# Performance work log

Measured on AMD Instinct MI355X. Metric: run time of the kernel, lower is better.

The kernel has to match this reference:

```python
import jax, jax.numpy as jnp
import numpy as np

B = 36          # fixed batch_size in source
T = 60          # time_window
DECAY = 0.3     # LIAF default decay
THRESH = 0.5    # LIAF default firing threshold


def conv3x3(x, W, b):
    # x: [B,C,H,W], W: [O,C,3,3], padding=1, stride=1
    y = jax.lax.conv_general_dilated(x, W, (1, 1), [(1, 1), (1, 1)],
                                     dimension_numbers=('NCHW', 'OIHW', 'NCHW'))
    return y + b[None, :, None, None]


def avgpool2(x):
    # 2x2 average pool, stride 2
    b, c, h, w = x.shape
    return x.reshape(b, c, h // 2, 2, w // 2, 2).mean(axis=(3, 5))


def liaf(u, spike, mem):
    # leaky-integrate with spike-gated reset, analog (ReLU) fire
    mem = mem * DECAY * (1.0 - spike) + u
    new_spike = (mem > THRESH).astype(mem.dtype)
    out = jax.nn.relu(mem)
    return new_spike, mem, out


def setup_inputs() -> dict:
    key = jax.random.key(0)
    ks = jax.random.split(key, 8)
    # DVS event frames in [0,3) so the >1 binarization keeps ~2/3 of pixels
    data = (jax.random.uniform(ks[0], (B, 2, 32, 32, T)) * 3.0).astype(jnp.float32)

    def w(k, shape, fan_in):
        return (jax.random.normal(k, shape) * (1.0 / np.sqrt(fan_in))).astype(jnp.float32)

    return dict(
        data=data,
        win=T,
        W0=w(ks[1], (64, 2, 3, 3), 2 * 9), b0=jnp.zeros((64,), jnp.float32),
        W1=w(ks[2], (128, 64, 3, 3), 64 * 9), b1=jnp.zeros((128,), jnp.float32),
        W2=w(ks[3], (128, 128, 3, 3), 128 * 9), b2=jnp.zeros((128,), jnp.float32),
        Wf1=w(ks[4], (256, 8192), 8192), bf1=jnp.zeros((256,), jnp.float32),
        Wf2=w(ks[5], (11, 256), 256), bf2=jnp.zeros((11,), jnp.float32),
    )


def reference(data, W0, b0, W1, b1, W2, b2, Wf1, bf1, Wf2, bf2, win):
    dtype = data.dtype
    z = lambda s: jnp.zeros(s, dtype)
    # (spike, mem) pairs for every LIAF cell + output-spike accumulator
    state0 = (
        (z((B, 64, 32, 32)), z((B, 64, 32, 32))),   # c0
        (z((B, 128, 32, 32)), z((B, 128, 32, 32))), # c1
        (z((B, 128, 16, 16)), z((B, 128, 16, 16))), # p1
        (z((B, 128, 16, 16)), z((B, 128, 16, 16))), # c2
        (z((B, 128, 8, 8)), z((B, 128, 8, 8))),     # p2
        (z((B, 256)), z((B, 256))),                 # h1
        (z((B, 11)), z((B, 11))),                   # h2
        z((B, 11)),                                 # sum of analog outputs
    )
    xs = jnp.moveaxis(data, -1, 0)[:win]

    def step(st, xt):
        c0, c1, p1, c2, p2, h1, h2, acc = st
        x = (xt > 1.0).astype(dtype)  # binarize accumulated frame
        s, m, out = liaf(conv3x3(x, W0, b0), *c0); c0 = (s, m)
        s, m, out = liaf(conv3x3(out, W1, b1), *c1); c1 = (s, m)
        s, m, out = liaf(avgpool2(out), *p1); p1 = (s, m)
        s, m, out = liaf(conv3x3(out, W2, b2), *c2); c2 = (s, m)
        s, m, out = liaf(avgpool2(out), *p2); p2 = (s, m)
        out = out.reshape(B, -1)  # [B, 8*8*128]
        s, m, out = liaf(out @ Wf1.T + bf1, *h1); h1 = (s, m)
        s, m, out = liaf(out @ Wf2.T + bf2, *h2); h2 = (s, m)
        return (c0, c1, p1, c2, p2, h1, h2, acc + out), None

    st_f, _ = jax.lax.scan(step, state0, xs)
    return st_f[-1] / T
```

## Files before the change

kernel.cpp:

```cpp
#include <hip/hip_runtime.h>

#define NB 36
#define NT 60

typedef __attribute__((ext_vector_type(8))) short short8;
typedef __attribute__((ext_vector_type(4))) float f32x4;

struct Params {
  const float *data;
  const float *W0, *b0, *W1, *b1, *W2, *b2, *Wf1, *bf1, *Wf2, *bf2;
  float *xb, *w0t;
  unsigned short *w1h, *w1l, *w2h, *w2l;
  unsigned int *xhl, *p1hl;
  float *outp2, *u1s;
  float *dm0, *dm1, *dmp1, *dm2, *dmp2, *dmh1, *dmh2;
  float *acc;
  float *zbase; int zn4;
};

__device__ __forceinline__ unsigned short bf16_rne(float v){
  unsigned int bits = __float_as_uint(v);
  unsigned int r = bits + 0x7FFFu + ((bits >> 16) & 1u);
  return (unsigned short)(r >> 16);
}
__device__ __forceinline__ unsigned int bf16pack(float v){
  unsigned short h = bf16_rne(v);
  float hf = __uint_as_float((unsigned int)h << 16);
  unsigned short l = bf16_rne(v - hf);
  return (unsigned int)h | ((unsigned int)l << 16);
}
__device__ __forceinline__ void unpack8(const unsigned int* q, short8& h8, short8& l8){
  unsigned int u[8];
  *(uint4*)&u[0] = *(const uint4*)q;
  *(uint4*)&u[4] = *(const uint4*)(q+4);
  #pragma unroll
  for(int i=0;i<8;i++){
    h8[i] = (short)(u[i] & 0xffffu);
    l8[i] = (short)(u[i] >> 16);
  }
}

__global__ void __launch_bounds__(256) k_prep(Params p){
  int gt  = blockIdx.x*256 + threadIdx.x;
  int STR = gridDim.x*256;
  if(gt < NB*11) p.acc[gt] = 0.f;
  for(int i=gt; i<p.zn4; i+=STR) ((float4*)p.zbase)[i] = make_float4(0.f,0.f,0.f,0.f);
  const int PLANE = 34*34;
  for(int i=gt; i<NT*NB*2*PLANE; i+=STR){
    int t   = i / (NB*2*PLANE);
    int rem = i % (NB*2*PLANE);
    int bc  = rem / PLANE;
    int pix = rem % PLANE;
    int ph = pix/34, pw = pix%34;
    float v = 0.f;
    if(ph>=1 && ph<=32 && pw>=1 && pw<=32){
      float d = p.data[((size_t)bc*1024 + (ph-1)*32 + (pw-1))*NT + t];
      v = (d > 1.0f) ? 1.0f : 0.0f;
    }
    p.xb[i] = v;
  }
  for(int i=gt; i<2*9*64; i+=STR){
    int co=i%64, rr=i/64; p.w0t[i] = p.W0[(co*2 + rr/9)*9 + rr%9];
  }
  for(int i=gt; i<128*576; i+=STR){
    int co = i/576, k = i%576;
    int cin = k/9, dd = k%9;
    unsigned int pk = bf16pack(p.W1[(co*64+cin)*9 + dd]);
    p.w1h[i]=(unsigned short)(pk&0xffffu); p.w1l[i]=(unsigned short)(pk>>16);
  }
  for(int i=gt; i<128*1152; i+=STR){
    int co = i/1152, k = i%1152;
    int cin = k/9, dd = k%9;
    unsigned int pk = bf16pack(p.W2[(co*128+cin)*9 + dd]);
    p.w2h[i]=(unsigned short)(pk&0xffffu); p.w2l[i]=(unsigned short)(pk>>16);
  }
}

template<int Cin,int Cout,int HW,int CO,int PX,int TY,int CS>
__global__ void __launch_bounds__(HW*TY)
k_conv0(const float* __restrict__ x, const float* __restrict__ wt,
        const float* __restrict__ bias, float* __restrict__ dm,
        unsigned int* __restrict__ outhl,
        const float* __restrict__ u1s, const float* __restrict__ bf1,
        const float* __restrict__ Wf2, const float* __restrict__ bf2,
        float* __restrict__ dmh1, float* __restrict__ dmh2,
        float* __restrict__ accv, int do_fc2)
{
  const int NCOG = Cout/CO;
  const int TH   = PX*TY;
  const int NHG  = HW/TH;
  const int NH4  = CO/4;
  const int NTHL = HW*TY;
  const int PIN  = HW+2;
  const int XR   = PX+2;
  int tile = blockIdx.x;
  int tid  = threadIdx.x;

  __shared__ __align__(16) float wl[CS*9*CO];
  __shared__ float xs[256];

  if(do_fc2 && tile < NB){
    int b = tile;
    int o = tid;
    float u = bf1[o];
    const float* pu = u1s + (size_t)b*256 + o;
    #pragma unroll
    for(int s=0;s<32;s++) u += pu[(size_t)s*NB*256];
    int idx = b*256 + o;
    float mem = dmh1[idx] + u;
    float xo = mem > 0.f ? mem : 0.f;
    dmh1[idx] = (mem > 0.5f) ? 0.f : 0.3f*mem;
    xs[o] = xo;
    __syncthreads();
    int w2id = o >> 6, ln = o & 63;
    for(int oo=w2id; oo<11; oo+=4){
      const float* wr = Wf2 + oo*256;
      float s = xs[ln]*wr[ln] + xs[ln+64]*wr[ln+64]
              + xs[ln+128]*wr[ln+128] + xs[ln+192]*wr[ln+192];
      #pragma unroll
      for(int off=32; off>0; off>>=1) s += __shfl_down(s, off, 64);
      if(ln==0){
        int i2 = b*11 + oo;
        float m2 = dmh2[i2] + s + bf2[oo];
        float ov = m2 > 0.f ? m2 : 0.f;
        dmh2[i2] = (m2 > 0.5f) ? 0.f : 0.3f*m2;
        accv[i2] += ov * (1.0f/60.0f);
      }
    }
  }

  int cog = tile % NCOG;
  int hg  = (tile/NCOG) % NHG;
  int b   = tile/(NCOG*NHG);
  int w0  = tid % HW;
  int ty  = tid / HW;
  int h0  = hg*TH + ty*PX;

  float accs[PX][CO];
  #pragma unroll
  for(int p=0;p<PX;p++)
    #pragma unroll
    for(int c=0;c<CO;c++) accs[p][c]=0.f;

  for(int cs=0; cs<Cin; cs+=CS){
    __syncthreads();
    for(int j=tid; j<CS*9*CO; j+=NTHL){
      int c  = j % CO;
      int rr = j / CO;
      wl[j] = wt[(cs*9 + rr)*Cout + cog*CO + c];
    }
    __syncthreads();

    for(int lc=0; lc<CS; lc++){
      const float* xc = x + ((size_t)b*Cin + cs + lc)*PIN*PIN + (size_t)h0*PIN + w0;
      float xv[XR][3];
      #pragma unroll
      for(int r=0;r<XR;r++)
        #pragma unroll
        for(int c=0;c<3;c++) xv[r][c] = xc[(size_t)r*PIN + c];
      const float4* w4 = (const float4*)(wl + lc*9*CO);
      #pragma unroll
      for(int dh=0;dh<3;dh++){
        #pragma unroll
        for(int g=0;g<NH4;g++){
          float4 wa = w4[(dh*3+0)*NH4+g];
          float4 wb = w4[(dh*3+1)*NH4+g];
          float4 wc = w4[(dh*3+2)*NH4+g];
          const float* A  = (const float*)&wa;
          const float* Bp = (const float*)&wb;
          const float* Cp = (const float*)&wc;
          #pragma unroll
          for(int cc=0;cc<4;cc++){
            #pragma unroll
            for(int px=0;px<PX;px++)
              accs[px][g*4+cc] += A[cc]*xv[px+dh][0] + Bp[cc]*xv[px+dh][1] + Cp[cc]*xv[px+dh][2];
          }
        }
      }
    }
  }

  int co0 = cog*CO;
  #pragma unroll
  for(int co=0; co<CO; co++){
    float bsv = bias[co0+co];
    const int OS = HW + 2;
    size_t plane = (size_t)(b*Cout + co0+co)*OS*OS;
    #pragma unroll
    for(int px=0; px<PX; px++){
      size_t idx = plane + (size_t)(h0+px+1)*OS + w0 + 1;
      float mem = dm[idx] + accs[px][co] + bsv;
      float ov = mem > 0.f ? mem : 0.f;
      dm[idx]  = (mem > 0.5f) ? 0.f : 0.3f*mem;
      outhl[idx] = bf16pack(ov);
    }
  }
}

__global__ void __launch_bounds__(256)
k_conv1(const unsigned int* __restrict__ xhl,
        const unsigned short* __restrict__ w1h, const unsigned short* __restrict__ w1l,
        const float* __restrict__ bias, float* __restrict__ dm,
        float* __restrict__ dmp, unsigned int* __restrict__ p1hl)
{
  __shared__ __align__(16) unsigned int ldsu[8192];
  unsigned short* Ah = (unsigned short*)ldsu;
  unsigned short* Al = (unsigned short*)(ldsu + 1280);
  unsigned int*   Xp = ldsu + 2560;

  int bid = blockIdx.x;
  int cog = bid & 1;
  int pxg = (bid>>1) & 7;
  int b   = bid >> 4;
  int tid = threadIdx.x;
  int wv  = tid >> 6, lane = tid & 63;
  int wm = wv & 1, wn = wv >> 1;
  int n = lane & 15, quad = lane >> 4;
  int r0 = pxg*4;

  f32x4 acc[2][4];
  #pragma unroll
  for(int mo=0;mo<2;mo++)
    #pragma unroll
    for(int no=0;no<4;no++) acc[mo][no] = (f32x4){0.f,0.f,0.f,0.f};

  int aco = tid >> 2;
  int aq  = tid & 3;
  const unsigned short* whp = w1h + (size_t)(cog*64 + aco)*576 + aq*8;
  const unsigned short* wlp = w1l + (size_t)(cog*64 + aco)*576 + aq*8;
  int sk  = tid >> 3;
  int pxq = tid & 7;
  int srow = pxq >> 1;
  int scol = (pxq & 1) * 16;
  int pxb  = pxq * 16;
  int skx  = sk ^ ((pxq & 3) << 3);

  uint4 wha = *(const uint4*)(whp);
  uint4 wla = *(const uint4*)(wlp);
  unsigned int tmp[16];
  {
    int cin = sk / 9;
    int dd  = sk - cin*9;
    int dh = dd/3, dw = dd - dh*3;
    const unsigned int* sx = xhl + ((size_t)(b*64 + cin)*34 + (r0 + srow + dh))*34 + scol + dw;
    #pragma unroll
    for(int i=0;i<16;i++) tmp[i] = sx[i];
  }

  for(int ch=0; ch<18; ch++){
    __syncthreads();
    *(uint4*)&Ah[aco*40 + aq*8] = wha;
    *(uint4*)&Al[aco*40 + aq*8] = wla;
    #pragma unroll
    for(int i=0;i<16;i++) Xp[(pxb+i)*44 + skx] = tmp[i];
    __syncthreads();

    if(ch+1 < 18){
      int k0n = (ch+1)*32;
      wha = *(const uint4*)(whp + k0n);
      wla = *(const uint4*)(wlp + k0n);
      int kg = k0n + sk;
      int cin = kg / 9;
      int dd  = kg - cin*9;
      int dh = dd/3, dw = dd - dh*3;
      const unsigned int* sx = xhl + ((size_t)(b*64 + cin)*34 + (r0 + srow + dh))*34 + scol + dw;
      #pragma unroll
      for(int i=0;i<16;i++) tmp[i] = sx[i];
    }

    short8 ahf[2], alf[2];
    #pragma unroll
    for(int mo=0;mo<2;mo++){
      int row = wm*32 + mo*16 + n;
      ahf[mo] = *(const short8*)&Ah[row*40 + quad*8];
      alf[mo] = *(const short8*)&Al[row*40 + quad*8];
    }
    #pragma unroll
    for(int no=0;no<4;no++){
      int prow = wn*64 + no*16 + n;
      short8 xhf, xlf;
      unpack8(&Xp[prow*44 + ((quad ^ no) & 3)*8], xhf, xlf);
      #pragma unroll
      for(int mo=0;mo<2;mo++){
        acc[mo][no] = __builtin_amdgcn_mfma_f32_16x16x32_bf16(ahf[mo], xhf, acc[mo][no],0,0,0);
        acc[mo][no] = __builtin_amdgcn_mfma_f32_16x16x32_bf16(ahf[mo], xlf, acc[mo][no],0,0,0);
        acc[mo][no] = __builtin_amdgcn_mfma_f32_16x16x32_bf16(alf[mo], xhf, acc[mo][no],0,0,0);
      }
    }
  }

  #pragma unroll
  for(int mo=0;mo<2;mo++){
    #pragma unroll
    for(int reg=0;reg<4;reg++){
      int co = cog*64 + wm*32 + mo*16 + quad*4 + reg;
      float bsv = bias[co];
      float o[4];
      #pragma unroll
      for(int no=0;no<4;no++){
        int r = r0 + wn*2 + (no>>1);
        int c = (no&1)*16 + n;
        size_t idx = (((size_t)b*128 + co)*32 + r)*32 + c;
        float mem = dm[idx] + acc[mo][no][reg] + bsv;
        o[no] = mem > 0.f ? mem : 0.f;
        dm[idx] = (mem > 0.5f) ? 0.f : 0.3f*mem;
      }
      #pragma unroll
      for(int pp=0; pp<2; pp++){
        float s = o[pp] + o[pp+2];
        s += __shfl_xor(s, 1, 64);
        if((n&1)==0){
          int pr = pxg*2 + wn;
          int pc = pp*8 + (n>>1);
          size_t pidx = (((size_t)b*128 + co)*18 + pr+1)*18 + pc+1;
          float pm = dmp[pidx] + s*0.25f;
          float pv = pm > 0.f ? pm : 0.f;
          dmp[pidx] = (pm > 0.5f) ? 0.f : 0.3f*pm;
          p1hl[pidx] = bf16pack(pv);
        }
      }
    }
  }
}

__global__ void __launch_bounds__(256)
k_conv2(const unsigned int* __restrict__ xhl,
        const unsigned short* __restrict__ w2h, const unsigned short* __restrict__ w2l,
        const float* __restrict__ bias, float* __restrict__ dm,
        float* __restrict__ dmp, float* __restrict__ outp)
{
  __shared__ __align__(16) unsigned int ldsu[5376];
  unsigned short* Ah = (unsigned short*)ldsu;
  unsigned short* Al = (unsigned short*)(ldsu + 1280);
  unsigned int*   Xp = ldsu + 2560;

  int bid = blockIdx.x;
  int cog = bid & 1;
  int pxg = (bid>>1) & 3;
  int b   = bid >> 3;
  int tid = threadIdx.x;
  int wv  = tid >> 6, lane = tid & 63;
  int wm = wv & 1, wn = wv >> 1;
  int n = lane & 15, quad = lane >> 4;
  int r0 = pxg*4;

  f32x4 acc[2][2];
  #pragma unroll
  for(int mo=0;mo<2;mo++)
    #pragma unroll
    for(int no=0;no<2;no++) acc[mo][no] = (f32x4){0.f,0.f,0.f,0.f};

  int aco = tid >> 2;
  int aq  = tid & 3;
  const unsigned short* whp = w2h + (size_t)(cog*64 + aco)*1152 + aq*8;
  const unsigned short* wlp = w2l + (size_t)(cog*64 + aco)*1152 + aq*8;
  int sk  = tid >> 3;
  int pxq = tid & 7;
  int srow = pxq >> 1;
  int scol = (pxq & 1) * 8;
  int pxb  = pxq * 8;
  int skx  = sk ^ ((pxq >> 1) << 3);

  uint4 wha = *(const uint4*)(whp);
  uint4 wla = *(const uint4*)(wlp);
  unsigned int tmp[8];
  {
    int cin = sk / 9;
    int dd  = sk - cin*9;
    int dh = dd/3, dw = dd - dh*3;
    const unsigned int* sx = xhl + ((size_t)(b*128 + cin)*18 + (r0 + srow + dh))*18 + scol + dw;
    #pragma unroll
    for(int i=0;i<8;i++) tmp[i] = sx[i];
  }

  for(int ch=0; ch<36; ch++){
    __syncthreads();
    *(uint4*)&Ah[aco*40 + aq*8] = wha;
    *(uint4*)&Al[aco*40 + aq*8] = wla;
    #pragma unroll
    for(int i=0;i<8;i++) Xp[(pxb+i)*44 + skx] = tmp[i];
    __syncthreads();

    if(ch+1 < 36){
      int k0n = (ch+1)*32;
      wha = *(const uint4*)(whp + k0n);
      wla = *(const uint4*)(wlp + k0n);
      int kg = k0n + sk;
      int cin = kg / 9;
      int dd  = kg - cin*9;
      int dh = dd/3, dw = dd - dh*3;
      const unsigned int* sx = xhl + ((size_t)(b*128 + cin)*18 + (r0 + srow + dh))*18 + scol + dw;
      #pragma unroll
      for(int i=0;i<8;i++) tmp[i] = sx[i];
    }

    short8 ahf[2], alf[2];
    #pragma unroll
    for(int mo=0;mo<2;mo++){
      int row = wm*32 + mo*16 + n;
      ahf[mo] = *(const short8*)&Ah[row*40 + quad*8];
      alf[mo] = *(const short8*)&Al[row*40 + quad*8];
    }
    #pragma unroll
    for(int no=0;no<2;no++){
      int prow = wn*32 + no*16 + n;
      short8 xhf, xlf;
      unpack8(&Xp[prow*44 + ((quad ^ (wn*2 + no)) & 3)*8], xhf, xlf);
      #pragma unroll
      for(int mo=0;mo<2;mo++){
        acc[mo][no] = __builtin_amdgcn_mfma_f32_16x16x32_bf16(ahf[mo], xhf, acc[mo][no],0,0,0);
        acc[mo][no] = __builtin_amdgcn_mfma_f32_16x16x32_bf16(ahf[mo], xlf, acc[mo][no],0,0,0);
        acc[mo][no] = __builtin_amdgcn_mfma_f32_16x16x32_bf16(alf[mo], xhf, acc[mo][no],0,0,0);
      }
    }
  }

  #pragma unroll
  for(int mo=0;mo<2;mo++){
    #pragma unroll
    for(int reg=0;reg<4;reg++){
      int co = cog*64 + wm*32 + mo*16 + quad*4 + reg;
      float bsv = bias[co];
      float o[2];
      #pragma unroll
      for(int no=0;no<2;no++){
        int r = r0 + wn*2 + no;
        int c = n;
        size_t idx = (((size_t)b*128 + co)*16 + r)*16 + c;
        float mem = dm[idx] + acc[mo][no][reg] + bsv;
        o[no] = mem > 0.f ? mem : 0.f;
        dm[idx] = (mem > 0.5f) ? 0.f : 0.3f*mem;
      }
      float s = o[0] + o[1];
      s += __shfl_xor(s, 1, 64);
      if((n&1)==0){
        int pr = pxg*2 + wn;
        int pc = n>>1;
        size_t pidx = (((size_t)b*128 + co)*8 + pr)*8 + pc;
        float pm = dmp[pidx] + s*0.25f;
        outp[pidx] = pm > 0.f ? pm : 0.f;
        dmp[pidx]  = (pm > 0.5f) ? 0.f : 0.3f*pm;
      }
    }
  }
}

__global__ void __launch_bounds__(256)
k_fc1(const float* __restrict__ X, const float* __restrict__ Wf,
      float* __restrict__ u1s){
  __shared__ __align__(16) float lds[4896];
  float* Wl = lds;
  float* Xl = lds + 32*68;
  const int tid = threadIdx.x;
  int ot = blockIdx.x & 7, ks = blockIdx.x >> 3;
  int o0 = ot*32, k0 = ks*256;
  int w_id = tid >> 6, lane = tid & 63;
  int o_l = lane & 7, bg = lane >> 3;
  float acc[4][5];
  #pragma unroll
  for(int i=0;i<4;i++)
    #pragma unroll
    for(int j=0;j<5;j++) acc[i][j]=0.f;

  for(int c=0; c<4; c++){
    int kb = k0 + c*64;
    __syncthreads();
    for(int idx=tid; idx<512; idx+=256){
      int r = idx >> 4, j = idx & 15;
      *(float4*)&Wl[r*68 + j*4] = *(const float4*)&Wf[(size_t)(o0+r)*8192 + kb + j*4];
    }
    for(int idx=tid; idx<640; idx+=256){
      int r = idx >> 4, j = idx & 15;
      float4 v = make_float4(0.f,0.f,0.f,0.f);
      if(r < NB) v = *(const float4*)&X[(size_t)r*8192 + kb + j*4];
      *(float4*)&Xl[r*68 + j*4] = v;
    }
    __syncthreads();
    #pragma unroll
    for(int c4=0; c4<4; c4++){
      int g = w_id*4 + c4;
      float4 wv[4], xv[5];
      #pragma unroll
      for(int oi=0;oi<4;oi++) wv[oi] = *(const float4*)&Wl[(o_l+8*oi)*68 + g*4];
      #pragma unroll
      for(int bi=0;bi<5;bi++) xv[bi] = *(const float4*)&Xl[(bg*5+bi)*68 + g*4];
      #pragma unroll
      for(int oi=0;oi<4;oi++)
        #pragma unroll
        for(int bi=0;bi<5;bi++)
          acc[oi][bi] += wv[oi].x*xv[bi].x + wv[oi].y*xv[bi].y
                       + wv[oi].z*xv[bi].z + wv[oi].w*xv[bi].w;
    }
  }
  __syncthreads();
  if(w_id > 0){
    float* r = lds + ((w_id-1)*64 + lane)*20;
    #pragma unroll
    for(int oi=0;oi<4;oi++)
      #pragma unroll
      for(int bi=0;bi<5;bi++) r[oi*5+bi] = acc[oi][bi];
  }
  __syncthreads();
  if(w_id == 0){
    #pragma unroll
    for(int wv=0;wv<3;wv++){
      float* r = lds + (wv*64 + lane)*20;
      #pragma unroll
      for(int oi=0;oi<4;oi++)
        #pragma unroll
        for(int bi=0;bi<5;bi++) acc[oi][bi] += r[oi*5+bi];
    }
    #pragma unroll
    for(int bi=0;bi<5;bi++){
      int b = bg*5 + bi;
      if(b < NB){
        #pragma unroll
        for(int oi=0;oi<4;oi++)
          u1s[((size_t)ks*NB + b)*256 + o0 + o_l + 8*oi] = acc[oi][bi];
      }
    }
  }
}

__global__ void __launch_bounds__(256)
k_fc2(const float* __restrict__ u1s, const float* __restrict__ bf1,
      const float* __restrict__ Wf2, const float* __restrict__ bf2,
      float* __restrict__ dmh1, float* __restrict__ dmh2, float* __restrict__ acc){
  __shared__ float xs[256];
  int b = blockIdx.x;
  int o = threadIdx.x;
  float u = bf1[o];
  const float* p = u1s + (size_t)b*256 + o;
  #pragma unroll
  for(int s=0;s<32;s++) u += p[(size_t)s*NB*256];
  int idx = b*256 + o;
  float mem = dmh1[idx] + u;
  float xo = mem > 0.f ? mem : 0.f;
  dmh1[idx] = (mem > 0.5f) ? 0.f : 0.3f*mem;
  xs[o] = xo;
  __syncthreads();
  int w_id = o >> 6, lane = o & 63;
  for(int oo=w_id; oo<11; oo+=4){
    const float* wr = Wf2 + oo*256;
    float s = xs[lane]*wr[lane] + xs[lane+64]*wr[lane+64]
            + xs[lane+128]*wr[lane+128] + xs[lane+192]*wr[lane+192];
    #pragma unroll
    for(int off=32; off>0; off>>=1) s += __shfl_down(s, off, 64);
    if(lane==0){
      int i2 = b*11 + oo;
      float m2 = dmh2[i2] + s + bf2[oo];
      float ov = m2 > 0.f ? m2 : 0.f;
      dmh2[i2] = (m2 > 0.5f) ? 0.f : 0.3f*m2;
      acc[i2] += ov * (1.0f/60.0f);
    }
  }
}

extern "C" void kernel_launch(void* const* d_in, const int* in_sizes, int n_in,
                              void* d_out, int out_size, void* d_ws, size_t ws_size,
                              hipStream_t stream) {
  Params p;
  p.data = (const float*)d_in[0];
  p.W0  = (const float*)d_in[2];  p.b0  = (const float*)d_in[3];
  p.W1  = (const float*)d_in[4];  p.b1  = (const float*)d_in[5];
  p.W2  = (const float*)d_in[6];  p.b2  = (const float*)d_in[7];
  p.Wf1 = (const float*)d_in[8];  p.bf1 = (const float*)d_in[9];
  p.Wf2 = (const float*)d_in[10]; p.bf2 = (const float*)d_in[11];
  p.acc = (float*)d_out;

  float* ws = (float*)d_ws;
  const size_t S_XB    = (size_t)NT*NB*2*34*34;
  const size_t S_W0T   = 2*9*64;
  const size_t S_W1S   = 128*576/2;
  const size_t S_W2S   = 128*1152/2;
  const size_t S_XHL   = (size_t)NB*64*34*34;
  const size_t S_P1HL  = (size_t)NB*128*18*18;
  const size_t S_OP2   = (size_t)NB*128*8*8;
  const size_t S_U1S   = (size_t)32*NB*256;
  const size_t S_DM0   = (size_t)NB*64*34*34;
  const size_t S_DM1   = (size_t)NB*128*32*32;
  const size_t S_DMP1  = (size_t)NB*128*18*18;
  const size_t S_DM2   = (size_t)NB*128*16*16;
  const size_t S_DMP2  = S_OP2;
  const size_t S_OH1   = (size_t)NB*256;

  p.xb    = ws;  ws += S_XB;
  p.w0t   = ws;  ws += S_W0T;
  p.w1h   = (unsigned short*)ws;  ws += S_W1S;
  p.w1l   = (unsigned short*)ws;  ws += S_W1S;
  p.w2h   = (unsigned short*)ws;  ws += S_W2S;
  p.w2l   = (unsigned short*)ws;  ws += S_W2S;
  p.zbase = ws;
  p.xhl   = (unsigned int*)ws;    ws += S_XHL;
  p.p1hl  = (unsigned int*)ws;    ws += S_P1HL;
  p.outp2 = ws;  ws += S_OP2;
  p.u1s   = ws;  ws += S_U1S;
  p.dm0   = ws;  ws += S_DM0;
  p.dm1   = ws;  ws += S_DM1;
  p.dmp1  = ws;  ws += S_DMP1;
  p.dm2   = ws;  ws += S_DM2;
  p.dmp2  = ws;  ws += S_DMP2;
  p.dmh1  = ws;  ws += S_OH1;
  p.dmh2  = ws;  ws += (size_t)NB*11;
  p.zn4   = (int)((ws - p.zbase) / 4);

  k_prep<<<dim3(1024), dim3(256), 0, stream>>>(p);
  for(int t=0; t<NT; t++){
    const float* xt = p.xb + (size_t)t*NB*2*34*34;
    k_conv0<2,64,32,8,4,8,2><<<dim3(288), dim3(256), 0, stream>>>(
        xt, p.w0t, p.b0, p.dm0, p.xhl,
        p.u1s, p.bf1, p.Wf2, p.bf2, p.dmh1, p.dmh2, p.acc, t > 0 ? 1 : 0);
    k_conv1<<<dim3(576), dim3(256), 0, stream>>>(
        p.xhl, p.w1h, p.w1l, p.b1, p.dm1, p.dmp1, p.p1hl);
    k_conv2<<<dim3(288), dim3(256), 0, stream>>>(
        p.p1hl, p.w2h, p.w2l, p.b2, p.dm2, p.dmp2, p.outp2);
    k_fc1<<<dim3(256), dim3(256), 0, stream>>>(p.outp2, p.Wf1, p.u1s);
  }
  k_fc2<<<dim3(36), dim3(256), 0, stream>>>(p.u1s, p.bf1, p.Wf2, p.bf2,
                                            p.dmh1, p.dmh2, p.acc);
}
```

Measured before the change: 6.044 ms.

## Pipeline timesteps by fusing conv0/fc1/fc2 into conv1 and conv2 launches

Each timestep now uses two launches instead of four. The fc1 of the previous step runs as extra blocks inside the conv1 grid, and conv0 of the next step plus fc2 of the previous step run as extra blocks in the conv2 grid. The first conv0 is hoisted before the loop, and the final fc1/fc2 run after it. This removes launch gaps and lets small stages overlap with the large convolutions. The cost is heterogeneous blocks sharing one LDS allocation, and register pressure set by the largest branch.

```diff
diff --git a/kernel.cpp b/kernel.cpp
--- a/kernel.cpp
+++ b/kernel.cpp
@@ -80,11 +80,7 @@
 __global__ void __launch_bounds__(HW*TY)
 k_conv0(const float* __restrict__ x, const float* __restrict__ wt,
         const float* __restrict__ bias, float* __restrict__ dm,
-        unsigned int* __restrict__ outhl,
-        const float* __restrict__ u1s, const float* __restrict__ bf1,
-        const float* __restrict__ Wf2, const float* __restrict__ bf2,
-        float* __restrict__ dmh1, float* __restrict__ dmh2,
-        float* __restrict__ accv, int do_fc2)
+        unsigned int* __restrict__ outhl)
 {
   const int NCOG = Cout/CO;
   const int TH   = PX*TY;
@@ -95,46 +91,14 @@
   const int XR   = PX+2;
   int tile = blockIdx.x;
   int tid  = threadIdx.x;
-
-  __shared__ __align__(16) float wl[CS*9*CO];
-  __shared__ float xs[256];
-
-  if(do_fc2 && tile < NB){
-    int b = tile;
-    int o = tid;
-    float u = bf1[o];
-    const float* pu = u1s + (size_t)b*256 + o;
-    #pragma unroll
-    for(int s=0;s<32;s++) u += pu[(size_t)s*NB*256];
-    int idx = b*256 + o;
-    float mem = dmh1[idx] + u;
-    float xo = mem > 0.f ? mem : 0.f;
-    dmh1[idx] = (mem > 0.5f) ? 0.f : 0.3f*mem;
-    xs[o] = xo;
-    __syncthreads();
-    int w2id = o >> 6, ln = o & 63;
-    for(int oo=w2id; oo<11; oo+=4){
-      const float* wr = Wf2 + oo*256;
-      float s = xs[ln]*wr[ln] + xs[ln+64]*wr[ln+64]
-              + xs[ln+128]*wr[ln+128] + xs[ln+192]*wr[ln+192];
-      #pragma unroll
-      for(int off=32; off>0; off>>=1) s += __shfl_down(s, off, 64);
-      if(ln==0){
-        int i2 = b*11 + oo;
-        float m2 = dmh2[i2] + s + bf2[oo];
-        float ov = m2 > 0.f ? m2 : 0.f;
-        dmh2[i2] = (m2 > 0.5f) ? 0.f : 0.3f*m2;
-        accv[i2] += ov * (1.0f/60.0f);
-      }
-    }
-  }
-
   int cog = tile % NCOG;
   int hg  = (tile/NCOG) % NHG;
   int b   = tile/(NCOG*NHG);
   int w0  = tid % HW;
   int ty  = tid / HW;
   int h0  = hg*TH + ty*PX;
+
+  __shared__ __align__(16) float wl[CS*9*CO];
 
   float accs[PX][CO];
   #pragma unroll
@@ -198,21 +162,101 @@
 }
 
 __global__ void __launch_bounds__(256)
-k_conv1(const unsigned int* __restrict__ xhl,
-        const unsigned short* __restrict__ w1h, const unsigned short* __restrict__ w1l,
-        const float* __restrict__ bias, float* __restrict__ dm,
-        float* __restrict__ dmp, unsigned int* __restrict__ p1hl)
+k_x1(const unsigned int* __restrict__ xhl,
+     const unsigned short* __restrict__ w1h, const unsigned short* __restrict__ w1l,
+     const float* __restrict__ bias, float* __restrict__ dm,
+     float* __restrict__ dmp, unsigned int* __restrict__ p1hl,
+     const float* __restrict__ X, const float* __restrict__ Wf,
+     float* __restrict__ u1s, int do_fc1)
 {
   __shared__ __align__(16) unsigned int ldsu[8192];
+  const int tid = threadIdx.x;
+  int bid = blockIdx.x;
+
+  if(bid >= 576){
+    if(!do_fc1) return;
+    float* lds = (float*)ldsu;
+    float* Wl = lds;
+    float* Xl = lds + 32*68;
+    int bq = bid - 576;
+    int ot = bq & 7, ks = bq >> 3;
+    int o0 = ot*32, k0 = ks*256;
+    int w_id = tid >> 6, lane = tid & 63;
+    int o_l = lane & 7, bg = lane >> 3;
+    float acc[4][5];
+    #pragma unroll
+    for(int i=0;i<4;i++)
+      #pragma unroll
+      for(int j=0;j<5;j++) acc[i][j]=0.f;
+
+    for(int c=0; c<4; c++){
+      int kb = k0 + c*64;
+      __syncthreads();
+      for(int idx=tid; idx<512; idx+=256){
+        int r = idx >> 4, j = idx & 15;
+        *(float4*)&Wl[r*68 + j*4] = *(const float4*)&Wf[(size_t)(o0+r)*8192 + kb + j*4];
+      }
+      for(int idx=tid; idx<640; idx+=256){
+        int r = idx >> 4, j = idx & 15;
+        float4 v = make_float4(0.f,0.f,0.f,0.f);
+        if(r < NB) v = *(const float4*)&X[(size_t)r*8192 + kb + j*4];
+        *(float4*)&Xl[r*68 + j*4] = v;
+      }
+      __syncthreads();
+      #pragma unroll
+      for(int c4=0; c4<4; c4++){
+        int g = w_id*4 + c4;
+        float4 wv[4], xv[5];
+        #pragma unroll
+        for(int oi=0;oi<4;oi++) wv[oi] = *(const float4*)&Wl[(o_l+8*oi)*68 + g*4];
+        #pragma unroll
+        for(int bi=0;bi<5;bi++) xv[bi] = *(const float4*)&Xl[(bg*5+bi)*68 + g*4];
+        #pragma unroll
+        for(int oi=0;oi<4;oi++)
+          #pragma unroll
+          for(int bi=0;bi<5;bi++)
+            acc[oi][bi] += wv[oi].x*xv[bi].x + wv[oi].y*xv[bi].y
+                         + wv[oi].z*xv[bi].z + wv[oi].w*xv[bi].w;
+      }
+    }
+    __syncthreads();
+    if(w_id > 0){
+      float* r = lds + ((w_id-1)*64 + lane)*20;
+      #pragma unroll
+      for(int oi=0;oi<4;oi++)
+        #pragma unroll
+        for(int bi=0;bi<5;bi++) r[oi*5+bi] = acc[oi][bi];
+    }
+    __syncthreads();
+    if(w_id == 0){
+      #pragma unroll
+      for(int wv=0;wv<3;wv++){
+        float* r = lds + (wv*64 + lane)*20;
+        #pragma unroll
+        for(int oi=0;oi<4;oi++)
+          #pragma unroll
+          for(int bi=0;bi<5;bi++) acc[oi][bi] += r[oi*5+bi];
+      }
+      #pragma unroll
+      for(int bi=0;bi<5;bi++){
+        int b = bg*5 + bi;
+        if(b < NB){
+          #pragma unroll
+          for(int oi=0;oi<4;oi++)
+            u1s[((size_t)ks*NB + b)*256 + o0 + o_l + 8*oi] = acc[oi][bi];
+        }
+      }
+    }
+    return;
+  }
+
   unsigned short* Ah = (unsigned short*)ldsu;
   unsigned short* Al = (unsigned short*)(ldsu + 1280);
   unsigned int*   Xp = ldsu + 2560;
 
-  int bid = blockIdx.x;
   int cog = bid & 1;
   int pxg = (bid>>1) & 7;
   int b   = bid >> 4;
-  int tid = threadIdx.x;
   int wv  = tid >> 6, lane = tid & 63;
   int wm = wv & 1, wn = wv >> 1;
   int n = lane & 15, quad = lane >> 4;
@@ -324,21 +368,131 @@
 }
 
 __global__ void __launch_bounds__(256)
-k_conv2(const unsigned int* __restrict__ xhl,
-        const unsigned short* __restrict__ w2h, const unsigned short* __restrict__ w2l,
-        const float* __restrict__ bias, float* __restrict__ dm,
-        float* __restrict__ dmp, float* __restrict__ outp)
+k_x2(const unsigned int* __restrict__ p1hl,
+     const unsigned short* __restrict__ w2h, const unsigned short* __restrict__ w2l,
+     const float* __restrict__ bias2, float* __restrict__ dm2,
+     float* __restrict__ dmp2, float* __restrict__ outp,
+     const float* __restrict__ xnext, const float* __restrict__ w0t,
+     const float* __restrict__ bias0, float* __restrict__ dm0,
+     unsigned int* __restrict__ xhl, int do_c0,
+     const float* __restrict__ u1s, const float* __restrict__ bf1,
+     const float* __restrict__ Wf2, const float* __restrict__ bf2,
+     float* __restrict__ dmh1, float* __restrict__ dmh2,
+     float* __restrict__ accv, int do_fc2)
 {
   __shared__ __align__(16) unsigned int ldsu[5376];
+  const int tid = threadIdx.x;
+  int bid = blockIdx.x;
+
+  if(bid >= 576){
+    if(!do_fc2) return;
+    float* xs = (float*)ldsu;
+    int b = bid - 576;
+    int o = tid;
+    float u = bf1[o];
+    const float* pu = u1s + (size_t)b*256 + o;
+    #pragma unroll
+    for(int s=0;s<32;s++) u += pu[(size_t)s*NB*256];
+    int idx = b*256 + o;
+    float mem = dmh1[idx] + u;
+    float xo = mem > 0.f ? mem : 0.f;
+    dmh1[idx] = (mem > 0.5f) ? 0.f : 0.3f*mem;
+    xs[o] = xo;
+    __syncthreads();
+    int w_id = o >> 6, ln = o & 63;
+    for(int oo=w_id; oo<11; oo+=4){
+      const float* wr = Wf2 + oo*256;
+      float s = xs[ln]*wr[ln] + xs[ln+64]*wr[ln+64]
+              + xs[ln+128]*wr[ln+128] + xs[ln+192]*wr[ln+192];
+      #pragma unroll
+      for(int off=32; off>0; off>>=1) s += __shfl_down(s, off, 64);
+      if(ln==0){
+        int i2 = b*11 + oo;
+        float m2 = dmh2[i2] + s + bf2[oo];
+        float ov = m2 > 0.f ? m2 : 0.f;
+        dmh2[i2] = (m2 > 0.5f) ? 0.f : 0.3f*m2;
+        accv[i2] += ov * (1.0f/60.0f);
+      }
+    }
+    return;
+  }
+
+  if(bid >= 288){
+    if(!do_c0) return;
+    float* wl = (float*)ldsu;
+    int tile = bid - 288;
+    int cog = tile & 7;
+    int b   = tile >> 3;
+    int w0  = tid & 31;
+    int ty  = tid >> 5;
+    int h0  = ty*4;
+
+    float accs[4][8];
+    #pragma unroll
+    for(int p=0;p<4;p++)
+      #pragma unroll
+      for(int c=0;c<8;c++) accs[p][c]=0.f;
+
+    if(tid < 144){
+      int c  = tid % 8;
+      int rr = tid / 8;
+      wl[tid] = w0t[rr*64 + cog*8 + c];
+    }
+    __syncthreads();
+
+    #pragma unroll
+    for(int lc=0; lc<2; lc++){
+      const float* xc = xnext + ((size_t)b*2 + lc)*34*34 + (size_t)h0*34 + w0;
+      float xv[6][3];
+      #pragma unroll
+      for(int r=0;r<6;r++)
+        #pragma unroll
+        for(int c=0;c<3;c++) xv[r][c] = xc[(size_t)r*34 + c];
+      const float4* w4 = (const float4*)(wl + lc*72);
+      #pragma unroll
+      for(int dh=0;dh<3;dh++){
+        #pragma unroll
+        for(int g=0;g<2;g++){
+          float4 wa = w4[(dh*3+0)*2+g];
+          float4 wb = w4[(dh*3+1)*2+g];
+          float4 wc = w4[(dh*3+2)*2+g];
+          const float* A  = (const float*)&wa;
+          const float* Bp = (const float*)&wb;
+          const float* Cp = (const float*)&wc;
+          #pragma unroll
+          for(int cc=0;cc<4;cc++){
+            #pragma unroll
+            for(int px=0;px<4;px++)
+              accs[px][g*4+cc] += A[cc]*xv[px+dh][0] + Bp[cc]*xv[px+dh][1] + Cp[cc]*xv[px+dh][2];
+          }
+        }
+      }
+    }
+
+    int co0 = cog*8;
+    #pragma unroll
+    for(int co=0; co<8; co++){
+      float bsv = bias0[co0+co];
+      size_t plane = (size_t)(b*64 + co0+co)*34*34;
+      #pragma unroll
+      for(int px=0; px<4; px++){
+        size_t idx = plane + (size_t)(h0+px+1)*34 + w0 + 1;
+        float mem = dm0[idx] + accs[px][co] + bsv;
+        float ov = mem > 0.f ? mem : 0.f;
+        dm0[idx]  = (mem > 0.5f) ? 0.f : 0.3f*mem;
+        xhl[idx] = bf16pack(ov);
+      }
+    }
+    return;
+  }
+
   unsigned short* Ah = (unsigned short*)ldsu;
   unsigned short* Al = (unsigned short*)(ldsu + 1280);
   unsigned int*   Xp = ldsu + 2560;
 
-  int bid = blockIdx.x;
   int cog = bid & 1;
   int pxg = (bid>>1) & 3;
   int b   = bid >> 3;
-  int tid = threadIdx.x;
   int wv  = tid >> 6, lane = tid & 63;
   int wm = wv & 1, wn = wv >> 1;
   int n = lane & 15, quad = lane >> 4;
@@ -368,7 +522,7 @@
     int cin = sk / 9;
     int dd  = sk - cin*9;
     int dh = dd/3, dw = dd - dh*3;
-    const unsigned int* sx = xhl + ((size_t)(b*128 + cin)*18 + (r0 + srow + dh))*18 + scol + dw;
+    const unsigned int* sx = p1hl + ((size_t)(b*128 + cin)*18 + (r0 + srow + dh))*18 + scol + dw;
     #pragma unroll
     for(int i=0;i<8;i++) tmp[i] = sx[i];
   }
@@ -389,7 +543,7 @@
       int cin = kg / 9;
       int dd  = kg - cin*9;
       int dh = dd/3, dw = dd - dh*3;
-      const unsigned int* sx = xhl + ((size_t)(b*128 + cin)*18 + (r0 + srow + dh))*18 + scol + dw;
+      const unsigned int* sx = p1hl + ((size_t)(b*128 + cin)*18 + (r0 + srow + dh))*18 + scol + dw;
       #pragma unroll
       for(int i=0;i<8;i++) tmp[i] = sx[i];
     }
@@ -420,16 +574,16 @@
     #pragma unroll
     for(int reg=0;reg<4;reg++){
       int co = cog*64 + wm*32 + mo*16 + quad*4 + reg;
-      float bsv = bias[co];
+      float bsv = bias2[co];
       float o[2];
       #pragma unroll
       for(int no=0;no<2;no++){
         int r = r0 + wn*2 + no;
         int c = n;
         size_t idx = (((size_t)b*128 + co)*16 + r)*16 + c;
-        float mem = dm[idx] + acc[mo][no][reg] + bsv;
+        float mem = dm2[idx] + acc[mo][no][reg] + bsv;
         o[no] = mem > 0.f ? mem : 0.f;
-        dm[idx] = (mem > 0.5f) ? 0.f : 0.3f*mem;
+        dm2[idx] = (mem > 0.5f) ? 0.f : 0.3f*mem;
       }
       float s = o[0] + o[1];
       s += __shfl_xor(s, 1, 64);
@@ -437,9 +591,9 @@
         int pr = pxg*2 + wn;
         int pc = n>>1;
         size_t pidx = (((size_t)b*128 + co)*8 + pr)*8 + pc;
-        float pm = dmp[pidx] + s*0.25f;
+        float pm = dmp2[pidx] + s*0.25f;
         outp[pidx] = pm > 0.f ? pm : 0.f;
-        dmp[pidx]  = (pm > 0.5f) ? 0.f : 0.3f*pm;
+        dmp2[pidx]  = (pm > 0.5f) ? 0.f : 0.3f*pm;
       }
     }
   }
@@ -605,17 +759,19 @@
   p.zn4   = (int)((ws - p.zbase) / 4);
 
   k_prep<<<dim3(1024), dim3(256), 0, stream>>>(p);
+  k_conv0<2,64,32,8,4,8,2><<<dim3(288), dim3(256), 0, stream>>>(
+      p.xb, p.w0t, p.b0, p.dm0, p.xhl);
   for(int t=0; t<NT; t++){
-    const float* xt = p.xb + (size_t)t*NB*2*34*34;
-    k_conv0<2,64,32,8,4,8,2><<<dim3(288), dim3(256), 0, stream>>>(
-        xt, p.w0t, p.b0, p.dm0, p.xhl,
+    k_x1<<<dim3(832), dim3(256), 0, stream>>>(
+        p.xhl, p.w1h, p.w1l, p.b1, p.dm1, p.dmp1, p.p1hl,
+        p.outp2, p.Wf1, p.u1s, t > 0 ? 1 : 0);
+    const float* xnext = p.xb + (size_t)(t+1)*NB*2*34*34;
+    k_x2<<<dim3(612), dim3(256), 0, stream>>>(
+        p.p1hl, p.w2h, p.w2l, p.b2, p.dm2, p.dmp2, p.outp2,
+        xnext, p.w0t, p.b0, p.dm0, p.xhl, t < NT-1 ? 1 : 0,
         p.u1s, p.bf1, p.Wf2, p.bf2, p.dmh1, p.dmh2, p.acc, t > 0 ? 1 : 0);
-    k_conv1<<<dim3(576), dim3(256), 0, stream>>>(
-        p.xhl, p.w1h, p.w1l, p.b1, p.dm1, p.dmp1, p.p1hl);
-    k_conv2<<<dim3(288), dim3(256), 0, stream>>>(
-        p.p1hl, p.w2h, p.w2l, p.b2, p.dm2, p.dmp2, p.outp2);
-    k_fc1<<<dim3(256), dim3(256), 0, stream>>>(p.outp2, p.Wf1, p.u1s);
-  }
+  }
+  k_fc1<<<dim3(256), dim3(256), 0, stream>>>(p.outp2, p.Wf1, p.u1s);
   k_fc2<<<dim3(36), dim3(256), 0, stream>>>(p.u1s, p.bf1, p.Wf2, p.bf2,
                                             p.dmh1, p.dmh2, p.acc);
 }
```

New measurement: 6.850 ms. +13.3%, slower.
